# Kernel tuning notes

Measured on AMD Instinct MI355X. Metric: run time of the kernel, lower is better.

## Reference

```python
import jax, jax.numpy as jnp
import numpy as np

B, N, H, T = 128, 512, 128, 4

def setup_inputs() -> dict:
    key = jax.random.key(0)
    ks = jax.random.split(key, 16)
    stdv = 1.0 / np.sqrt(H)
    u = lambda k, shape: jax.random.uniform(k, shape, jnp.float32, -stdv, stdv)
    return {
        "A": jax.random.uniform(ks[0], (B, N, N), jnp.float32),
        "hidden": jax.random.normal(ks[1], (B, N, H), jnp.float32),
        "b_ah": u(ks[2], (H,)),
        "w_z": u(ks[3], (H, H)), "b_wz": u(ks[4], (H,)),
        "u_z": u(ks[5], (H, H)), "b_uz": u(ks[6], (H,)),
        "w_r": u(ks[7], (H, H)), "b_wr": u(ks[8], (H,)),
        "u_r": u(ks[9], (H, H)), "b_ur": u(ks[10], (H,)),
        "w": u(ks[11], (H, H)), "b_w": u(ks[12], (H,)),
        "u": u(ks[13], (H, H)), "b_u": u(ks[14], (H,)),
    }

def reference(A, hidden, b_ah, w_z, b_wz, u_z, b_uz, w_r, b_wr, u_r, b_ur, w, b_w, u, b_u):
    # A: [B,N,N], hidden: [B,N,H]. F.linear(x, W, b) == x @ W.T + b
    def cell(h, _):
        # a = A^T @ h + b_ah  -> [B,N,H]
        a = jnp.einsum('bmn,bmh->bnh', A, h) + b_ah
        z = jax.nn.sigmoid(a @ w_z.T + b_wz + h @ u_z.T + b_uz)
        r = jax.nn.sigmoid(a @ w_r.T + b_wr + h @ u_r.T + b_ur)
        c = jnp.tanh(a @ w.T + b_w + (r * h) @ u.T + b_u)
        h_t = (1.0 - z) * h + z * c
        return h_t, None
    h_out, _ = jax.lax.scan(cell, hidden, None, length=T)
    return h_out
```

## Files before the change

### kernel.cpp

```cpp
#include <hip/hip_runtime.h>
#include <hip/hip_fp16.h>

#define BB 128
#define NN 512
#define HH 128
#define TT 4

typedef _Float16 f16;
typedef _Float16 half8 __attribute__((ext_vector_type(8)));
typedef float floatx4 __attribute__((ext_vector_type(4)));

__device__ __forceinline__ void split1(float x, f16& hi, f16& lo) {
  hi = (f16)x;
  lo = (f16)(x - (float)hi);
}


__global__ void k_wsplit(const float* __restrict__ wz, const float* __restrict__ uz,
                         const float* __restrict__ wr, const float* __restrict__ ur,
                         const float* __restrict__ wc, const float* __restrict__ uc,
                         f16* __restrict__ whi, f16* __restrict__ wlo) {
  int mat = blockIdx.x >> 6;
  int idx = ((blockIdx.x & 63) << 8) + threadIdx.x;
  const float* src = mat==0?wz : mat==1?uz : mat==2?wr : mat==3?ur : mat==4?wc : uc;
  float v = src[idx] * 16.0f;
  f16 hi, lo; split1(v, hi, lo);
  whi[mat*16384 + idx] = hi;
  wlo[mat*16384 + idx] = lo;
}

__global__ void k_bsum(const float* __restrict__ bwz, const float* __restrict__ buz,
                       const float* __restrict__ bwr, const float* __restrict__ bur,
                       const float* __restrict__ bw,  const float* __restrict__ bu,
                       float* __restrict__ bias3) {
  int b = blockIdx.x, j = threadIdx.x;
  bias3[b*HH + j] = b==0 ? bwz[j]+buz[j] : (b==1 ? bwr[j]+bur[j] : bw[j]+bu[j]);
}

__global__ void k_copy_h0(const float* __restrict__ hin, float* __restrict__ h) {
  int v = blockIdx.x * 256 + threadIdx.x;
  ((float4*)h)[v] = ((const float4*)hin)[v];
}


__global__ __launch_bounds__(256) void k_biggemm(const float* __restrict__ A,
                                                 const float* __restrict__ h,
                                                 const float* __restrict__ b_ah,
                                                 float* __restrict__ a32) {
  __shared__ __align__(16) f16 Ah[128*64], Al[128*64], Hh[128*64], Hl[128*64];
  const int b = blockIdx.y, n0 = blockIdx.x * 128, tid = threadIdx.x;
  const int w = tid >> 6, L = tid & 63, quad = L >> 4, l16 = L & 15;
  const int rowsel = tid >> 5, colsel = tid & 31;
  const float* Ab = A + (size_t)b * NN * NN;
  const float* hb = h + (size_t)b * NN * HH;
  const floatx4 zero = {0.f, 0.f, 0.f, 0.f};
  floatx4 acc[2][8];
  for (int sr = 0; sr < 2; sr++) for (int sc = 0; sc < 8; sc++) acc[sr][sc] = zero;

  for (int mc = 0; mc < NN; mc += 64) {
    float4 va[8], vh[8];
#pragma unroll
    for (int i = 0; i < 8; i++) {
      int mm = rowsel * 8 + i;
      va[i] = *(const float4*)(Ab + (size_t)(mc + mm) * NN + n0 + colsel * 4);
      vh[i] = *(const float4*)(hb + (size_t)(mc + mm) * HH + colsel * 4);
    }
#pragma unroll
    for (int q = 0; q < 4; q++) {
      int c = colsel * 4 + q;
      half8 avh, avl, hvh, hvl;
#pragma unroll
      for (int i = 0; i < 8; i++) {
        f16 hi, lo;
        split1(((const float*)&va[i])[q], hi, lo); avh[i] = hi; avl[i] = lo;
        split1(((const float*)&vh[i])[q], hi, lo); hvh[i] = hi; hvl[i] = lo;
      }
      int blk = (rowsel ^ (c & 7)) * 8;
      *(half8*)&Ah[c*64 + blk] = avh;  *(half8*)&Al[c*64 + blk] = avl;
      *(half8*)&Hh[c*64 + blk] = hvh;  *(half8*)&Hl[c*64 + blk] = hvl;
    }
    __syncthreads();
#pragma unroll
    for (int ks = 0; ks < 2; ks++) {
      const int kb = ks * 4 + quad;
      half8 afh[2], afl[2], bfh[8], bfl[8];
      for (int sr = 0; sr < 2; sr++) {
        int c = w*32 + sr*16 + l16, o = c*64 + ((kb ^ (c & 7)) * 8);
        afh[sr] = *(const half8*)&Ah[o];
        afl[sr] = *(const half8*)&Al[o];
      }
      for (int sc = 0; sc < 8; sc++) {
        int c = sc*16 + l16, o = c*64 + ((kb ^ (c & 7)) * 8);
        bfh[sc] = *(const half8*)&Hh[o];
        bfl[sc] = *(const half8*)&Hl[o];
      }
      for (int sr = 0; sr < 2; sr++)
        for (int sc = 0; sc < 8; sc++) {
          acc[sr][sc] = __builtin_amdgcn_mfma_f32_16x16x32_f16(afh[sr], bfh[sc], acc[sr][sc], 0, 0, 0);
          acc[sr][sc] = __builtin_amdgcn_mfma_f32_16x16x32_f16(afh[sr], bfl[sc], acc[sr][sc], 0, 0, 0);
          acc[sr][sc] = __builtin_amdgcn_mfma_f32_16x16x32_f16(afl[sr], bfh[sc], acc[sr][sc], 0, 0, 0);
        }
    }
    __syncthreads();
  }
  float bah[8];
  for (int sc = 0; sc < 8; sc++) bah[sc] = b_ah[sc*16 + l16];
  float* ab = a32 + (size_t)b * NN * HH;
#pragma unroll
  for (int sr = 0; sr < 2; sr++)
    for (int rg = 0; rg < 4; rg++) {
      const int row = n0 + w*32 + sr*16 + quad*4 + rg;
      for (int sc = 0; sc < 8; sc++)
        ab[(size_t)row*HH + sc*16 + l16] = acc[sr][sc][rg] + bah[sc];
    }
}

__global__ __launch_bounds__(256, 2) void k_gates(const float* __restrict__ a32,
                                                  float* __restrict__ h,
                                                  const f16* __restrict__ whi,
                                                  const f16* __restrict__ wlo,
                                                  const float* __restrict__ bias3) {
  __shared__ __align__(16) f16 rhh[128*136], rhl[128*136];
  const int row0 = blockIdx.x << 7, tid = threadIdx.x;
  const int w = tid >> 6, L = tid & 63, quad = L >> 4, l16 = L & 15;
  const float* ap[2]; const float* hp[2];
  for (int sr = 0; sr < 2; sr++) {
    int r = row0 + w*32 + sr*16 + l16;
    ap[sr] = a32 + (size_t)r * HH;
    hp[sr] = h + (size_t)r * HH;
  }
  half8 afh[2][4], afl[2][4];
#pragma unroll
  for (int sr = 0; sr < 2; sr++)
#pragma unroll
    for (int ks = 0; ks < 4; ks++) {
      const int ko = ks*32 + quad*8;
      float4 p = *(const float4*)(ap[sr] + ko);
      float4 q2 = *(const float4*)(ap[sr] + ko + 4);
      const float* v = (const float*)&p;
      const float* v2 = (const float*)&q2;
      for (int i = 0; i < 4; i++) { f16 hi, lo; split1(v[i],  hi, lo); afh[sr][ks][i]   = hi; afl[sr][ks][i]   = lo; }
      for (int i = 0; i < 4; i++) { f16 hi, lo; split1(v2[i], hi, lo); afh[sr][ks][i+4] = hi; afl[sr][ks][i+4] = lo; }
    }
  const floatx4 zero = {0.f, 0.f, 0.f, 0.f};
  const f16* Wz_h = whi;            const f16* Wz_l = wlo;
  const f16* Uz_h = whi + 16384;    const f16* Uz_l = wlo + 16384;
  const f16* Wr_h = whi + 2*16384;  const f16* Wr_l = wlo + 2*16384;
  const f16* Ur_h = whi + 3*16384;  const f16* Ur_l = wlo + 3*16384;
  const f16* Wc_h = whi + 4*16384;  const f16* Wc_l = wlo + 4*16384;
  const f16* Uc_h = whi + 5*16384;  const f16* Uc_l = wlo + 5*16384;

  floatx4 racc[2][8], zacc[2][8];
  for (int sr = 0; sr < 2; sr++)
    for (int sc = 0; sc < 8; sc++) { racc[sr][sc] = zero; zacc[sr][sc] = zero; }
#pragma unroll
  for (int ks = 0; ks < 4; ks++) {
    const int ko = ks*32 + quad*8;
    half8 hfh[2], hfl[2];
    for (int sr = 0; sr < 2; sr++) {
      float4 p = *(const float4*)(hp[sr] + ko);
      float4 q2 = *(const float4*)(hp[sr] + ko + 4);
      const float* v = (const float*)&p; const float* v2 = (const float*)&q2;
      for (int i = 0; i < 4; i++) { f16 hi, lo; split1(v[i],  hi, lo); hfh[sr][i]   = hi; hfl[sr][i]   = lo; }
      for (int i = 0; i < 4; i++) { f16 hi, lo; split1(v2[i], hi, lo); hfh[sr][i+4] = hi; hfl[sr][i+4] = lo; }
    }
#pragma unroll
    for (int sc = 0; sc < 8; sc++) {
      const int wo = (sc*16 + l16)*HH + ko;
      half8 wrh = *(const half8*)(Wr_h + wo), wrl = *(const half8*)(Wr_l + wo);
      half8 urh = *(const half8*)(Ur_h + wo), url = *(const half8*)(Ur_l + wo);
      half8 wzh = *(const half8*)(Wz_h + wo), wzl = *(const half8*)(Wz_l + wo);
      half8 uzh = *(const half8*)(Uz_h + wo), uzl = *(const half8*)(Uz_l + wo);
      for (int sr = 0; sr < 2; sr++) {
        racc[sr][sc] = __builtin_amdgcn_mfma_f32_16x16x32_f16(afh[sr][ks], wrh, racc[sr][sc], 0, 0, 0);
        racc[sr][sc] = __builtin_amdgcn_mfma_f32_16x16x32_f16(afh[sr][ks], wrl, racc[sr][sc], 0, 0, 0);
        racc[sr][sc] = __builtin_amdgcn_mfma_f32_16x16x32_f16(afl[sr][ks], wrh, racc[sr][sc], 0, 0, 0);
        racc[sr][sc] = __builtin_amdgcn_mfma_f32_16x16x32_f16(hfh[sr], urh, racc[sr][sc], 0, 0, 0);
        racc[sr][sc] = __builtin_amdgcn_mfma_f32_16x16x32_f16(hfh[sr], url, racc[sr][sc], 0, 0, 0);
        racc[sr][sc] = __builtin_amdgcn_mfma_f32_16x16x32_f16(hfl[sr], urh, racc[sr][sc], 0, 0, 0);
        zacc[sr][sc] = __builtin_amdgcn_mfma_f32_16x16x32_f16(afh[sr][ks], wzh, zacc[sr][sc], 0, 0, 0);
        zacc[sr][sc] = __builtin_amdgcn_mfma_f32_16x16x32_f16(afh[sr][ks], wzl, zacc[sr][sc], 0, 0, 0);
        zacc[sr][sc] = __builtin_amdgcn_mfma_f32_16x16x32_f16(afl[sr][ks], wzh, zacc[sr][sc], 0, 0, 0);
        zacc[sr][sc] = __builtin_amdgcn_mfma_f32_16x16x32_f16(hfh[sr], uzh, zacc[sr][sc], 0, 0, 0);
        zacc[sr][sc] = __builtin_amdgcn_mfma_f32_16x16x32_f16(hfh[sr], uzl, zacc[sr][sc], 0, 0, 0);
        zacc[sr][sc] = __builtin_amdgcn_mfma_f32_16x16x32_f16(hfl[sr], uzh, zacc[sr][sc], 0, 0, 0);
      }
    }
  }
  {
    float brv[8];
    for (int sc = 0; sc < 8; sc++) brv[sc] = bias3[128 + sc*16 + l16];
#pragma unroll
    for (int sr = 0; sr < 2; sr++)
#pragma unroll
      for (int rg = 0; rg < 4; rg++) {
        const int lrow = w*32 + sr*16 + quad*4 + rg;
        const float* hrow = h + (size_t)(row0 + lrow)*HH;
        for (int sc = 0; sc < 8; sc++) {
          const int col = sc*16 + l16;
          float pr = racc[sr][sc][rg] * 0.0625f + brv[sc];
          float rv = 1.f / (1.f + expf(-pr));
          float rhv = rv * hrow[col];
          f16 hi, lo; split1(rhv, hi, lo);
          rhh[lrow*136 + col] = hi;
          rhl[lrow*136 + col] = lo;
        }
      }
  }
  asm volatile("s_waitcnt lgkmcnt(0)" ::: "memory");

  floatx4 cacc[2][8];
  for (int sr = 0; sr < 2; sr++) for (int sc = 0; sc < 8; sc++) cacc[sr][sc] = zero;
#pragma unroll
  for (int ks = 0; ks < 4; ks++) {
    const int ko = ks*32 + quad*8;
    half8 rfh[2], rfl[2];
    for (int sr = 0; sr < 2; sr++) {
      int o = (w*32 + sr*16 + l16)*136 + ko;
      rfh[sr] = *(const half8*)&rhh[o];
      rfl[sr] = *(const half8*)&rhl[o];
    }
#pragma unroll
    for (int sc = 0; sc < 8; sc++) {
      const int wo = (sc*16 + l16)*HH + ko;
      half8 wh = *(const half8*)(Wc_h + wo), wl = *(const half8*)(Wc_l + wo);
      half8 uh = *(const half8*)(Uc_h + wo), ul = *(const half8*)(Uc_l + wo);
      for (int sr = 0; sr < 2; sr++) {
        cacc[sr][sc] = __builtin_amdgcn_mfma_f32_16x16x32_f16(afh[sr][ks], wh, cacc[sr][sc], 0, 0, 0);
        cacc[sr][sc] = __builtin_amdgcn_mfma_f32_16x16x32_f16(afh[sr][ks], wl, cacc[sr][sc], 0, 0, 0);
        cacc[sr][sc] = __builtin_amdgcn_mfma_f32_16x16x32_f16(afl[sr][ks], wh, cacc[sr][sc], 0, 0, 0);
        cacc[sr][sc] = __builtin_amdgcn_mfma_f32_16x16x32_f16(rfh[sr], uh, cacc[sr][sc], 0, 0, 0);
        cacc[sr][sc] = __builtin_amdgcn_mfma_f32_16x16x32_f16(rfh[sr], ul, cacc[sr][sc], 0, 0, 0);
        cacc[sr][sc] = __builtin_amdgcn_mfma_f32_16x16x32_f16(rfl[sr], uh, cacc[sr][sc], 0, 0, 0);
      }
    }
  }
  float bzv[8], bcv[8];
  for (int sc = 0; sc < 8; sc++) {
    bzv[sc] = bias3[sc*16 + l16];
    bcv[sc] = bias3[256 + sc*16 + l16];
  }
#pragma unroll
  for (int sr = 0; sr < 2; sr++)
#pragma unroll
    for (int rg = 0; rg < 4; rg++) {
      const int lrow = w*32 + sr*16 + quad*4 + rg;
      float* hrow = h + (size_t)(row0 + lrow)*HH;
      for (int sc = 0; sc < 8; sc++) {
        const int col = sc*16 + l16;
        float pz = zacc[sr][sc][rg] * 0.0625f + bzv[sc];
        float zv = 1.f / (1.f + expf(-pz));
        float cv = tanhf(cacc[sr][sc][rg] * 0.0625f + bcv[sc]);
        float hv = hrow[col];
        hrow[col] = hv + zv*(cv - hv);
      }
    }
}

extern "C" void kernel_launch(void* const* d_in, const int* in_sizes, int n_in,
                              void* d_out, int out_size, void* d_ws, size_t ws_size,
                              hipStream_t stream) {
  const float* A      = (const float*)d_in[0];
  const float* hidden = (const float*)d_in[1];
  const float* b_ah   = (const float*)d_in[2];
  const float* w_z = (const float*)d_in[3];  const float* b_wz = (const float*)d_in[4];
  const float* u_z = (const float*)d_in[5];  const float* b_uz = (const float*)d_in[6];
  const float* w_r = (const float*)d_in[7];  const float* b_wr = (const float*)d_in[8];
  const float* u_r = (const float*)d_in[9];  const float* b_ur = (const float*)d_in[10];
  const float* w   = (const float*)d_in[11]; const float* b_w  = (const float*)d_in[12];
  const float* u   = (const float*)d_in[13]; const float* b_u  = (const float*)d_in[14];

  float* h = (float*)d_out;
  char* ws = (char*)d_ws;
  float* a32  = (float*)ws;
  f16*   whi  = (f16*)(ws + 33554432);
  f16*   wlo  = (f16*)(ws + 33751040);
  float* bias3= (float*)(ws + 33947648);

  k_wsplit<<<384, 256, 0, stream>>>(w_z, u_z, w_r, u_r, w, u, whi, wlo);
  k_bsum<<<3, HH, 0, stream>>>(b_wz, b_uz, b_wr, b_ur, b_w, b_u, bias3);
  k_copy_h0<<<8192, 256, 0, stream>>>(hidden, h);

  for (int t = 0; t < TT; t++) {
    k_biggemm<<<dim3(4, BB), 256, 0, stream>>>(A, h, b_ah, a32);
    k_gates<<<512, 256, 0, stream>>>(a32, h, whi, wlo, bias3);
  }
}
```

Baseline: 992.6 us.

## Restructure gates kernel into column-tiled passes to cut accumulator register pressure

Preloads the h fragments (hi/lo split) once for all k-steps, alongside the a fragments. The r-gate computation now runs in two column halves, and the z and c gates are computed together in four column quarters. This keeps fewer accumulators live at once: previously 32 floatx4 accumulators were live for r and z, then 16 for c. The aim is to avoid spills and sustain occupancy at launch_bounds(256,2), at the cost of holding more input fragments in registers and using non-unrolled outer loops.

```diff
diff --git a/kernel.cpp b/kernel.cpp
--- a/kernel.cpp
+++ b/kernel.cpp
@@ -129,7 +129,7 @@
     ap[sr] = a32 + (size_t)r * HH;
     hp[sr] = h + (size_t)r * HH;
   }
-  half8 afh[2][4], afl[2][4];
+  half8 afh[2][4], afl[2][4], hfh[2][4], hfl[2][4];
 #pragma unroll
   for (int sr = 0; sr < 2; sr++)
 #pragma unroll
@@ -141,6 +141,12 @@
       const float* v2 = (const float*)&q2;
       for (int i = 0; i < 4; i++) { f16 hi, lo; split1(v[i],  hi, lo); afh[sr][ks][i]   = hi; afl[sr][ks][i]   = lo; }
       for (int i = 0; i < 4; i++) { f16 hi, lo; split1(v2[i], hi, lo); afh[sr][ks][i+4] = hi; afl[sr][ks][i+4] = lo; }
+      float4 hpv = *(const float4*)(hp[sr] + ko);
+      float4 hqv = *(const float4*)(hp[sr] + ko + 4);
+      const float* hv1 = (const float*)&hpv;
+      const float* hv2 = (const float*)&hqv;
+      for (int i = 0; i < 4; i++) { f16 hi, lo; split1(hv1[i], hi, lo); hfh[sr][ks][i]   = hi; hfl[sr][ks][i]   = lo; }
+      for (int i = 0; i < 4; i++) { f16 hi, lo; split1(hv2[i], hi, lo); hfh[sr][ks][i+4] = hi; hfl[sr][ks][i+4] = lo; }
     }
   const floatx4 zero = {0.f, 0.f, 0.f, 0.f};
   const f16* Wz_h = whi;            const f16* Wz_l = wlo;
@@ -150,111 +156,108 @@
   const f16* Wc_h = whi + 4*16384;  const f16* Wc_l = wlo + 4*16384;
   const f16* Uc_h = whi + 5*16384;  const f16* Uc_l = wlo + 5*16384;
 
-  floatx4 racc[2][8], zacc[2][8];
-  for (int sr = 0; sr < 2; sr++)
-    for (int sc = 0; sc < 8; sc++) { racc[sr][sc] = zero; zacc[sr][sc] = zero; }
-#pragma unroll
-  for (int ks = 0; ks < 4; ks++) {
-    const int ko = ks*32 + quad*8;
-    half8 hfh[2], hfl[2];
-    for (int sr = 0; sr < 2; sr++) {
-      float4 p = *(const float4*)(hp[sr] + ko);
-      float4 q2 = *(const float4*)(hp[sr] + ko + 4);
-      const float* v = (const float*)&p; const float* v2 = (const float*)&q2;
-      for (int i = 0; i < 4; i++) { f16 hi, lo; split1(v[i],  hi, lo); hfh[sr][i]   = hi; hfl[sr][i]   = lo; }
-      for (int i = 0; i < 4; i++) { f16 hi, lo; split1(v2[i], hi, lo); hfh[sr][i+4] = hi; hfl[sr][i+4] = lo; }
-    }
-#pragma unroll
-    for (int sc = 0; sc < 8; sc++) {
-      const int wo = (sc*16 + l16)*HH + ko;
-      half8 wrh = *(const half8*)(Wr_h + wo), wrl = *(const half8*)(Wr_l + wo);
-      half8 urh = *(const half8*)(Ur_h + wo), url = *(const half8*)(Ur_l + wo);
-      half8 wzh = *(const half8*)(Wz_h + wo), wzl = *(const half8*)(Wz_l + wo);
-      half8 uzh = *(const half8*)(Uz_h + wo), uzl = *(const half8*)(Uz_l + wo);
-      for (int sr = 0; sr < 2; sr++) {
-        racc[sr][sc] = __builtin_amdgcn_mfma_f32_16x16x32_f16(afh[sr][ks], wrh, racc[sr][sc], 0, 0, 0);
-        racc[sr][sc] = __builtin_amdgcn_mfma_f32_16x16x32_f16(afh[sr][ks], wrl, racc[sr][sc], 0, 0, 0);
-        racc[sr][sc] = __builtin_amdgcn_mfma_f32_16x16x32_f16(afl[sr][ks], wrh, racc[sr][sc], 0, 0, 0);
-        racc[sr][sc] = __builtin_amdgcn_mfma_f32_16x16x32_f16(hfh[sr], urh, racc[sr][sc], 0, 0, 0);
-        racc[sr][sc] = __builtin_amdgcn_mfma_f32_16x16x32_f16(hfh[sr], url, racc[sr][sc], 0, 0, 0);
-        racc[sr][sc] = __builtin_amdgcn_mfma_f32_16x16x32_f16(hfl[sr], urh, racc[sr][sc], 0, 0, 0);
-        zacc[sr][sc] = __builtin_amdgcn_mfma_f32_16x16x32_f16(afh[sr][ks], wzh, zacc[sr][sc], 0, 0, 0);
-        zacc[sr][sc] = __builtin_amdgcn_mfma_f32_16x16x32_f16(afh[sr][ks], wzl, zacc[sr][sc], 0, 0, 0);
-        zacc[sr][sc] = __builtin_amdgcn_mfma_f32_16x16x32_f16(afl[sr][ks], wzh, zacc[sr][sc], 0, 0, 0);
-        zacc[sr][sc] = __builtin_amdgcn_mfma_f32_16x16x32_f16(hfh[sr], uzh, zacc[sr][sc], 0, 0, 0);
-        zacc[sr][sc] = __builtin_amdgcn_mfma_f32_16x16x32_f16(hfh[sr], uzl, zacc[sr][sc], 0, 0, 0);
-        zacc[sr][sc] = __builtin_amdgcn_mfma_f32_16x16x32_f16(hfl[sr], uzh, zacc[sr][sc], 0, 0, 0);
-      }
-    }
-  }
-  {
-    float brv[8];
-    for (int sc = 0; sc < 8; sc++) brv[sc] = bias3[128 + sc*16 + l16];
-#pragma unroll
-    for (int sr = 0; sr < 2; sr++)
-#pragma unroll
-      for (int rg = 0; rg < 4; rg++) {
-        const int lrow = w*32 + sr*16 + quad*4 + rg;
-        const float* hrow = h + (size_t)(row0 + lrow)*HH;
-        for (int sc = 0; sc < 8; sc++) {
-          const int col = sc*16 + l16;
-          float pr = racc[sr][sc][rg] * 0.0625f + brv[sc];
+#pragma unroll 1
+  for (int scT = 0; scT < 2; scT++) {
+    floatx4 racc[2][4];
+    for (int sr = 0; sr < 2; sr++) for (int si = 0; si < 4; si++) racc[sr][si] = zero;
+#pragma unroll
+    for (int ks = 0; ks < 4; ks++) {
+      const int ko = ks*32 + quad*8;
+#pragma unroll
+      for (int si = 0; si < 4; si++) {
+        const int wo = ((scT*4 + si)*16 + l16)*HH + ko;
+        half8 wh = *(const half8*)(Wr_h + wo), wl = *(const half8*)(Wr_l + wo);
+        half8 uh = *(const half8*)(Ur_h + wo), ul = *(const half8*)(Ur_l + wo);
+#pragma unroll
+        for (int sr = 0; sr < 2; sr++) {
+          racc[sr][si] = __builtin_amdgcn_mfma_f32_16x16x32_f16(afh[sr][ks], wh, racc[sr][si], 0, 0, 0);
+          racc[sr][si] = __builtin_amdgcn_mfma_f32_16x16x32_f16(afh[sr][ks], wl, racc[sr][si], 0, 0, 0);
+          racc[sr][si] = __builtin_amdgcn_mfma_f32_16x16x32_f16(afl[sr][ks], wh, racc[sr][si], 0, 0, 0);
+          racc[sr][si] = __builtin_amdgcn_mfma_f32_16x16x32_f16(hfh[sr][ks], uh, racc[sr][si], 0, 0, 0);
+          racc[sr][si] = __builtin_amdgcn_mfma_f32_16x16x32_f16(hfh[sr][ks], ul, racc[sr][si], 0, 0, 0);
+          racc[sr][si] = __builtin_amdgcn_mfma_f32_16x16x32_f16(hfl[sr][ks], uh, racc[sr][si], 0, 0, 0);
+        }
+      }
+    }
+#pragma unroll
+    for (int si = 0; si < 4; si++) {
+      const int col = (scT*4 + si)*16 + l16;
+      const float brv = bias3[128 + col];
+#pragma unroll
+      for (int sr = 0; sr < 2; sr++)
+#pragma unroll
+        for (int rg = 0; rg < 4; rg++) {
+          const int lrow = w*32 + sr*16 + quad*4 + rg;
+          const float* hrow = h + (size_t)(row0 + lrow)*HH;
+          float pr = racc[sr][si][rg] * 0.0625f + brv;
           float rv = 1.f / (1.f + expf(-pr));
           float rhv = rv * hrow[col];
           f16 hi, lo; split1(rhv, hi, lo);
           rhh[lrow*136 + col] = hi;
           rhl[lrow*136 + col] = lo;
         }
-      }
+    }
   }
   asm volatile("s_waitcnt lgkmcnt(0)" ::: "memory");
 
-  floatx4 cacc[2][8];
-  for (int sr = 0; sr < 2; sr++) for (int sc = 0; sc < 8; sc++) cacc[sr][sc] = zero;
-#pragma unroll
-  for (int ks = 0; ks < 4; ks++) {
-    const int ko = ks*32 + quad*8;
-    half8 rfh[2], rfl[2];
-    for (int sr = 0; sr < 2; sr++) {
-      int o = (w*32 + sr*16 + l16)*136 + ko;
-      rfh[sr] = *(const half8*)&rhh[o];
-      rfl[sr] = *(const half8*)&rhl[o];
-    }
-#pragma unroll
-    for (int sc = 0; sc < 8; sc++) {
-      const int wo = (sc*16 + l16)*HH + ko;
-      half8 wh = *(const half8*)(Wc_h + wo), wl = *(const half8*)(Wc_l + wo);
-      half8 uh = *(const half8*)(Uc_h + wo), ul = *(const half8*)(Uc_l + wo);
+#pragma unroll 1
+  for (int scT = 0; scT < 4; scT++) {
+    floatx4 zacc[2][2], cacc[2][2];
+    for (int sr = 0; sr < 2; sr++)
+      for (int si = 0; si < 2; si++) { zacc[sr][si] = zero; cacc[sr][si] = zero; }
+#pragma unroll
+    for (int ks = 0; ks < 4; ks++) {
+      const int ko = ks*32 + quad*8;
+      half8 rfh[2], rfl[2];
+#pragma unroll
       for (int sr = 0; sr < 2; sr++) {
-        cacc[sr][sc] = __builtin_amdgcn_mfma_f32_16x16x32_f16(afh[sr][ks], wh, cacc[sr][sc], 0, 0, 0);
-        cacc[sr][sc] = __builtin_amdgcn_mfma_f32_16x16x32_f16(afh[sr][ks], wl, cacc[sr][sc], 0, 0, 0);
-        cacc[sr][sc] = __builtin_amdgcn_mfma_f32_16x16x32_f16(afl[sr][ks], wh, cacc[sr][sc], 0, 0, 0);
-        cacc[sr][sc] = __builtin_amdgcn_mfma_f32_16x16x32_f16(rfh[sr], uh, cacc[sr][sc], 0, 0, 0);
-        cacc[sr][sc] = __builtin_amdgcn_mfma_f32_16x16x32_f16(rfh[sr], ul, cacc[sr][sc], 0, 0, 0);
-        cacc[sr][sc] = __builtin_amdgcn_mfma_f32_16x16x32_f16(rfl[sr], uh, cacc[sr][sc], 0, 0, 0);
-      }
-    }
-  }
-  float bzv[8], bcv[8];
-  for (int sc = 0; sc < 8; sc++) {
-    bzv[sc] = bias3[sc*16 + l16];
-    bcv[sc] = bias3[256 + sc*16 + l16];
-  }
-#pragma unroll
-  for (int sr = 0; sr < 2; sr++)
-#pragma unroll
-    for (int rg = 0; rg < 4; rg++) {
-      const int lrow = w*32 + sr*16 + quad*4 + rg;
-      float* hrow = h + (size_t)(row0 + lrow)*HH;
-      for (int sc = 0; sc < 8; sc++) {
-        const int col = sc*16 + l16;
-        float pz = zacc[sr][sc][rg] * 0.0625f + bzv[sc];
-        float zv = 1.f / (1.f + expf(-pz));
-        float cv = tanhf(cacc[sr][sc][rg] * 0.0625f + bcv[sc]);
-        float hv = hrow[col];
-        hrow[col] = hv + zv*(cv - hv);
-      }
-    }
+        int o = (w*32 + sr*16 + l16)*136 + ko;
+        rfh[sr] = *(const half8*)&rhh[o];
+        rfl[sr] = *(const half8*)&rhl[o];
+      }
+#pragma unroll
+      for (int si = 0; si < 2; si++) {
+        const int wo = ((scT*2 + si)*16 + l16)*HH + ko;
+        half8 wzh = *(const half8*)(Wz_h + wo), wzl = *(const half8*)(Wz_l + wo);
+        half8 uzh = *(const half8*)(Uz_h + wo), uzl = *(const half8*)(Uz_l + wo);
+        half8 wch = *(const half8*)(Wc_h + wo), wcl = *(const half8*)(Wc_l + wo);
+        half8 uch = *(const half8*)(Uc_h + wo), ucl = *(const half8*)(Uc_l + wo);
+#pragma unroll
+        for (int sr = 0; sr < 2; sr++) {
+          zacc[sr][si] = __builtin_amdgcn_mfma_f32_16x16x32_f16(afh[sr][ks], wzh, zacc[sr][si], 0, 0, 0);
+          zacc[sr][si] = __builtin_amdgcn_mfma_f32_16x16x32_f16(afh[sr][ks], wzl, zacc[sr][si], 0, 0, 0);
+          zacc[sr][si] = __builtin_amdgcn_mfma_f32_16x16x32_f16(afl[sr][ks], wzh, zacc[sr][si], 0, 0, 0);
+          zacc[sr][si] = __builtin_amdgcn_mfma_f32_16x16x32_f16(hfh[sr][ks], uzh, zacc[sr][si], 0, 0, 0);
+          zacc[sr][si] = __builtin_amdgcn_mfma_f32_16x16x32_f16(hfh[sr][ks], uzl, zacc[sr][si], 0, 0, 0);
+          zacc[sr][si] = __builtin_amdgcn_mfma_f32_16x16x32_f16(hfl[sr][ks], uzh, zacc[sr][si], 0, 0, 0);
+          cacc[sr][si] = __builtin_amdgcn_mfma_f32_16x16x32_f16(afh[sr][ks], wch, cacc[sr][si], 0, 0, 0);
+          cacc[sr][si] = __builtin_amdgcn_mfma_f32_16x16x32_f16(afh[sr][ks], wcl, cacc[sr][si], 0, 0, 0);
+          cacc[sr][si] = __builtin_amdgcn_mfma_f32_16x16x32_f16(afl[sr][ks], wch, cacc[sr][si], 0, 0, 0);
+          cacc[sr][si] = __builtin_amdgcn_mfma_f32_16x16x32_f16(rfh[sr], uch, cacc[sr][si], 0, 0, 0);
+          cacc[sr][si] = __builtin_amdgcn_mfma_f32_16x16x32_f16(rfh[sr], ucl, cacc[sr][si], 0, 0, 0);
+          cacc[sr][si] = __builtin_amdgcn_mfma_f32_16x16x32_f16(rfl[sr], uch, cacc[sr][si], 0, 0, 0);
+        }
+      }
+    }
+#pragma unroll
+    for (int si = 0; si < 2; si++) {
+      const int col = (scT*2 + si)*16 + l16;
+      const float bzv = bias3[col];
+      const float bcv = bias3[256 + col];
+#pragma unroll
+      for (int sr = 0; sr < 2; sr++)
+#pragma unroll
+        for (int rg = 0; rg < 4; rg++) {
+          const int lrow = w*32 + sr*16 + quad*4 + rg;
+          float* hrow = h + (size_t)(row0 + lrow)*HH;
+          float pz = zacc[sr][si][rg] * 0.0625f + bzv;
+          float zv = 1.f / (1.f + expf(-pz));
+          float cv = tanhf(cacc[sr][si][rg] * 0.0625f + bcv);
+          float hv = hrow[col];
+          hrow[col] = hv + zv*(cv - hv);
+        }
+    }
+  }
 }
 
 extern "C" void kernel_launch(void* const* d_in, const int* in_sizes, int n_in,
```

New measurement: 983.4 us. No clear change (-0.9%).
